# Kernel optimization log

Measured on AMD Instinct MI355X. Metric: run time of the kernel, lower is better.

## Reference

```python
import jax, jax.numpy as jnp
import numpy as np

HEADS = 8
DIM_HEAD = 64
DIM = 512
KERNEL = 33
SCALE = DIM_HEAD ** -0.5


def setup_inputs() -> dict:
    key = jax.random.key(0)
    k1, k2, k3, k4, k5, k6 = jax.random.split(key, 6)
    b, n = 2, 2048
    inner = HEADS * DIM_HEAD
    x = jax.random.normal(k1, (b, n, DIM), dtype=jnp.float32)
    mask = jax.random.uniform(k2, (b, n)) < 0.9
    W_qkv = jax.random.normal(k3, (DIM, inner * 3), dtype=jnp.float32) / np.sqrt(DIM)
    W_out = jax.random.normal(k4, (inner, DIM), dtype=jnp.float32) / np.sqrt(inner)
    b_out = jax.random.normal(k5, (DIM,), dtype=jnp.float32) * 0.01
    # depthwise Conv2d(heads, heads, (K,1), groups=heads) weight: (O=heads, I/groups=1, K, 1)
    conv_w = jax.random.normal(k6, (HEADS, 1, KERNEL, 1), dtype=jnp.float32) / np.sqrt(KERNEL)
    return {"x": x, "mask": mask, "W_qkv": W_qkv, "W_out": W_out,
            "b_out": b_out, "conv_w": conv_w}


def reference(x, mask, W_qkv, W_out, b_out, conv_w):
    b, n, _ = x.shape
    h, d = HEADS, DIM_HEAD
    qkv = (x @ W_qkv).reshape(b, n, 3, h, d)          # chunk(3) then (h d) split
    q = qkv[:, :, 0].transpose(0, 2, 1, 3)            # b h n d
    k = qkv[:, :, 1].transpose(0, 2, 1, 3)
    v = qkv[:, :, 2].transpose(0, 2, 1, 3)
    dots = jnp.einsum('bhid,bhjd->bhij', q, k) * SCALE
    mask_value = -jnp.finfo(dots.dtype).max
    dots = jnp.where(mask[:, None, None, :], dots, mask_value)
    attn = jax.nn.softmax(dots, axis=-1)
    out = jnp.einsum('bhij,bhjd->bhid', attn, v)      # b h n d
    # depthwise residual conv over sequence axis (height), per head
    pad = KERNEL // 2
    res = jax.lax.conv_general_dilated(
        v, conv_w, window_strides=(1, 1), padding=((pad, pad), (0, 0)),
        dimension_numbers=('NCHW', 'OIHW', 'NCHW'), feature_group_count=h)
    out = out + res
    out = out.transpose(0, 2, 1, 3).reshape(b, n, h * d)  # b n (h d)
    out = out @ W_out + b_out
    out = jnp.where(mask[:, :, None], out, 0.0)
    return out
```

## Files before the change

kernel.cpp:

```cpp
#include <hip/hip_runtime.h>
#include <float.h>

#define BATCH 2
#define SEQ   2048
#define HEADS 8
#define DHEAD 64
#define DIMM  512
#define NQKV  1536
#define QK_SCALE 0.125f

#define QKV_ELEMS ((size_t)BATCH * HEADS * SEQ * DHEAD)

typedef __bf16 bf16x8 __attribute__((ext_vector_type(8)));
typedef float  f32x4  __attribute__((ext_vector_type(4)));

__device__ __forceinline__ unsigned short bfbits(float f) {
  __bf16 h = (__bf16)f;
  return *(unsigned short*)&h;
}
__device__ __forceinline__ float bf2f(unsigned short u) {
  return __uint_as_float((unsigned)u << 16);
}

__global__ __launch_bounds__(1024) void prep_mask(const void* __restrict__ mraw,
                                                  float* __restrict__ maskf,
                                                  unsigned* __restrict__ kmaxn) {
  __shared__ int f_bf16, f_f32, f_gt1, f_oddnz;
  const int t = threadIdx.x;
  if (t < 16) kmaxn[t] = 0u;
  if (t == 0) { f_bf16 = 0; f_f32 = 0; f_gt1 = 0; f_oddnz = 0; }
  __syncthreads();
  const unsigned int* w = (const unsigned int*)mraw;
  unsigned int v = w[t];
  if (v == 0x3f803f80u) f_bf16 = 1;
  if (v == 0x3f800000u) f_f32 = 1;
  if (v > 1u)           f_gt1 = 1;
  if ((t & 1) && v != 0u) f_oddnz = 1;
  __syncthreads();
  int mode;
  if (f_bf16)       mode = 4;
  else if (f_f32)   mode = 3;
  else if (f_gt1)   mode = 1;
  else if (!f_oddnz) mode = 2;
  else              mode = 0;
  for (int i = t; i < BATCH * SEQ; i += 1024) {
    bool keep;
    if (mode == 4)      keep = ((const unsigned short*)mraw)[i] != 0;
    else if (mode == 3) keep = ((const float*)mraw)[i] != 0.f;
    else if (mode == 1) keep = ((const unsigned char*)mraw)[i] != 0;
    else if (mode == 2) keep = w[2 * i] != 0u;
    else                keep = w[i] != 0u;
    maskf[i] = keep ? 1.f : 0.f;
  }
}

__global__ __launch_bounds__(256) void transpose_w(const float* __restrict__ W,
                                                   unsigned short* __restrict__ Wt,
                                                   int K, int N) {
  __shared__ float T[64][65];
  const int t = threadIdx.x;
  const int n0 = blockIdx.x * 64, k0 = blockIdx.y * 64;
  {
    int r0 = t >> 4, c4 = t & 15;
#pragma unroll
    for (int rr = 0; rr < 4; ++rr) {
      int r = r0 + rr * 16;
      float4 v = *(const float4*)(W + (size_t)(k0 + r) * N + n0 + c4 * 4);
      T[r][c4 * 4 + 0] = v.x; T[r][c4 * 4 + 1] = v.y;
      T[r][c4 * 4 + 2] = v.z; T[r][c4 * 4 + 3] = v.w;
    }
  }
  __syncthreads();
  {
    int n = t >> 2, kc = t & 3;
    union { unsigned short u[16]; int4 v[2]; } p;
#pragma unroll
    for (int i = 0; i < 16; ++i) p.u[i] = bfbits(T[kc * 16 + i][n]);
    int4* dst = (int4*)(Wt + (size_t)(n0 + n) * K + k0 + kc * 16);
    dst[0] = p.v[0]; dst[1] = p.v[1];
  }
}

__global__ __launch_bounds__(256) void gemm_qkv_mfma(
    const float* __restrict__ X, const unsigned short* __restrict__ Wt,
    unsigned short* __restrict__ Qbf, unsigned short* __restrict__ Kbf,
    unsigned short* __restrict__ Vt) {
  __shared__ __align__(16) unsigned char Al[128 * 128];
  __shared__ __align__(16) unsigned char Bl[64 * 128];
  const int tid = threadIdx.x;
  const int lane = tid & 63;
  const int w = tid >> 6;
  const int l15 = lane & 15, g = lane >> 4;
  const int wr = w >> 1, wc = w & 1;
  int bid = blockIdx.x;
  int lid = (bid & 7) * 96 + (bid >> 3);
  int by = lid / 24, bx = lid - by * 24;
  const int m0 = by * 128;

  f32x4 acc[4][2] = {};
  const int srow = tid >> 3, scg = tid & 7;
  const int rsw = (l15 & 7) << 4;

  for (int k0 = 0; k0 < DIMM; k0 += 64) {
    __syncthreads();
#pragma unroll
    for (int it = 0; it < 4; ++it) {
      int row = srow + it * 32;
      int sw = (row & 7) << 4;
      const float* asrc = X + (size_t)(m0 + row) * DIMM + k0 + scg * 8;
      float4 a0 = *(const float4*)asrc;
      float4 a1 = *(const float4*)(asrc + 4);
      union { unsigned short u[8]; int4 v; } pk;
      pk.u[0] = bfbits(a0.x); pk.u[1] = bfbits(a0.y);
      pk.u[2] = bfbits(a0.z); pk.u[3] = bfbits(a0.w);
      pk.u[4] = bfbits(a1.x); pk.u[5] = bfbits(a1.y);
      pk.u[6] = bfbits(a1.z); pk.u[7] = bfbits(a1.w);
      *(int4*)(Al + row * 128 + ((scg * 16) ^ sw)) = pk.v;
      if (it < 2) {
        *(int4*)(Bl + row * 128 + ((scg * 16) ^ sw)) =
            *(const int4*)(Wt + (size_t)(bx * 64 + row) * DIMM + k0 + scg * 8);
      }
    }
    __syncthreads();
#pragma unroll
    for (int ks = 0; ks < 2; ++ks) {
      bf16x8 af[4], bfr[2];
#pragma unroll
      for (int mi = 0; mi < 4; ++mi)
        af[mi] = *(const bf16x8*)(Al + (wr * 64 + mi * 16 + l15) * 128 +
                                  ((ks * 64 + g * 16) ^ rsw));
#pragma unroll
      for (int nj = 0; nj < 2; ++nj)
        bfr[nj] = *(const bf16x8*)(Bl + (wc * 32 + nj * 16 + l15) * 128 +
                                   ((ks * 64 + g * 16) ^ rsw));
#pragma unroll
      for (int mi = 0; mi < 4; ++mi)
#pragma unroll
        for (int nj = 0; nj < 2; ++nj)
          acc[mi][nj] = __builtin_amdgcn_mfma_f32_16x16x32_bf16(
              af[mi], bfr[nj], acc[mi][nj], 0, 0, 0);
    }
  }
  const int chunk = bx >> 3;
  const int bb = m0 >> 11;
#pragma unroll
  for (int nj = 0; nj < 2; ++nj) {
    int col = (bx & 7) * 64 + wc * 32 + nj * 16 + l15;
    int hh = col >> 6, dd = col & 63;
#pragma unroll
    for (int mi = 0; mi < 4; ++mi) {
      int ii0 = (m0 & (SEQ - 1)) + wr * 64 + mi * 16 + g * 4;
      if (chunk == 2) {
        union { unsigned short u[4]; ushort4 v; } pk;
#pragma unroll
        for (int r = 0; r < 4; ++r) pk.u[r] = bfbits(acc[mi][nj][r]);
        *(ushort4*)(Vt + ((size_t)(bb * HEADS + hh) * DHEAD + dd) * SEQ + ii0) = pk.v;
      } else {
        unsigned short* dst = (chunk == 0) ? Qbf : Kbf;
        float sc = (chunk == 0) ? QK_SCALE : 1.f;
#pragma unroll
        for (int r = 0; r < 4; ++r)
          dst[((size_t)(bb * HEADS + hh) * SEQ + ii0 + r) * DHEAD + dd] =
              bfbits(acc[mi][nj][r] * sc);
      }
    }
  }
}

__global__ __launch_bounds__(256) void knorm(const unsigned short* __restrict__ Kbf,
                                             unsigned* __restrict__ kmaxn) {
  int row = blockIdx.x * 256 + threadIdx.x;
  const bf16x8* kr = (const bf16x8*)(Kbf + (size_t)row * DHEAD);
  float n2 = 0.f;
#pragma unroll
  for (int c = 0; c < 8; ++c) {
    bf16x8 v = kr[c];
#pragma unroll
    for (int i = 0; i < 8; ++i) { float f = (float)v[i]; n2 += f * f; }
  }
#pragma unroll
  for (int d = 1; d < 64; d <<= 1) n2 = fmaxf(n2, __shfl_xor(n2, d));
  if ((threadIdx.x & 63) == 0)
    atomicMax(kmaxn + (row >> 11), __float_as_uint(n2));
}

__global__ __launch_bounds__(256) void attn_split(const unsigned short* __restrict__ Qbf,
                                                  const unsigned short* __restrict__ Kbf,
                                                  const unsigned short* __restrict__ Vt,
                                                  const float* __restrict__ maskf,
                                                  const unsigned* __restrict__ kmaxn,
                                                  unsigned short* __restrict__ Po,
                                                  float* __restrict__ LSE) {
  __shared__ __align__(16) unsigned char Ks[8192];
  __shared__ __align__(16) unsigned char Vs[8192];
  __shared__ __align__(16) unsigned char Ps[8192];
  __shared__ float skm[64];
  __shared__ float qns[64];

  const int tid = threadIdx.x;
  const int lane = tid & 63;
  const int w = tid >> 6;
  const int l15 = lane & 15, g = lane >> 4;

  int fid = blockIdx.x;
  int lid = (fid & 7) * 128 + (fid >> 3);
  const int bh = lid >> 6;
  const int rem = lid & 63;
  const int qb = rem >> 1;
  const int half = rem & 1;
  const int bb = bh >> 3;

  const unsigned short* Qg = Qbf + ((size_t)bh * SEQ + qb * 64) * DHEAD;
  const unsigned short* Kg = Kbf + (size_t)bh * SEQ * DHEAD;
  const unsigned short* Vg = Vt  + (size_t)bh * DHEAD * SEQ;

  bf16x8 qf0, qf1;
  {
    const unsigned char* qrow = (const unsigned char*)(Qg + (size_t)(w * 16 + l15) * DHEAD);
    qf0 = *(const bf16x8*)(qrow + g * 16);
    qf1 = *(const bf16x8*)(qrow + 64 + g * 16);
  }
  {
    float qn2 = 0.f;
#pragma unroll
    for (int i = 0; i < 8; ++i) {
      float a = (float)qf0[i]; qn2 += a * a;
      float b = (float)qf1[i]; qn2 += b * b;
    }
    qn2 += __shfl_xor(qn2, 16);
    qn2 += __shfl_xor(qn2, 32);
    if (g == 0) qns[w * 16 + l15] = qn2;
  }
  __syncthreads();
  const float kmax2 = __uint_as_float(kmaxn[bh]);
  float B[4];
#pragma unroll
  for (int r = 0; r < 4; ++r) B[r] = sqrtf(qns[w * 16 + g * 4 + r] * kmax2);

  f32x4 o[4];
  float lsum[4] = {0.f, 0.f, 0.f, 0.f};
#pragma unroll
  for (int j = 0; j < 4; ++j) { o[j] = (f32x4){0.f, 0.f, 0.f, 0.f}; }

  const int sm = tid >> 2;
  const int sc = (tid & 3) * 32;
  const int ssw = (sm & 7) << 4;
  const int rsw = (l15 & 7) << 4;

  const int kt0 = half * 16;
  for (int kt = kt0; kt < kt0 + 16; ++kt) {
    __syncthreads();
    {
      const unsigned char* ksrc =
          (const unsigned char*)(Kg + (size_t)kt * 64 * DHEAD) + sm * 128 + sc;
      const unsigned char* vsrc =
          (const unsigned char*)(Vg + (size_t)sm * SEQ + kt * 64) + sc;
      *(int4*)(Ks + sm * 128 + ((sc)      ^ ssw)) = *(const int4*)(ksrc);
      *(int4*)(Ks + sm * 128 + ((sc + 16) ^ ssw)) = *(const int4*)(ksrc + 16);
      *(int4*)(Vs + sm * 128 + ((sc)      ^ ssw)) = *(const int4*)(vsrc);
      *(int4*)(Vs + sm * 128 + ((sc + 16) ^ ssw)) = *(const int4*)(vsrc + 16);
      if (tid < 64) skm[tid] = maskf[bb * SEQ + kt * 64 + tid];
    }
    __syncthreads();

    f32x4 s[4];
#pragma unroll
    for (int j = 0; j < 4; ++j) {
      const unsigned char* krow = Ks + (16 * j + l15) * 128;
      bf16x8 kf0 = *(const bf16x8*)(krow + ((g * 16)      ^ rsw));
      bf16x8 kf1 = *(const bf16x8*)(krow + ((64 + g * 16) ^ rsw));
      f32x4 z = (f32x4){0.f, 0.f, 0.f, 0.f};
      z = __builtin_amdgcn_mfma_f32_16x16x32_bf16(qf0, kf0, z, 0, 0, 0);
      z = __builtin_amdgcn_mfma_f32_16x16x32_bf16(qf1, kf1, z, 0, 0, 0);
      s[j] = z;
    }

    float km0 = skm[l15], km1 = skm[16 + l15], km2 = skm[32 + l15], km3 = skm[48 + l15];
#pragma unroll
    for (int r = 0; r < 4; ++r) {
      float p0 = __expf(s[0][r] - B[r]) * km0;
      float p1 = __expf(s[1][r] - B[r]) * km1;
      float p2 = __expf(s[2][r] - B[r]) * km2;
      float p3 = __expf(s[3][r] - B[r]) * km3;
      lsum[r] += (p0 + p1) + (p2 + p3);
      int pm = w * 16 + g * 4 + r;
      unsigned char* prow = Ps + pm * 128;
      int psw = (pm & 7) << 4;
      *(__bf16*)(prow + ((2 * (l15)      ) ^ psw)) = (__bf16)p0;
      *(__bf16*)(prow + ((2 * (16 + l15) ) ^ psw)) = (__bf16)p1;
      *(__bf16*)(prow + ((2 * (32 + l15) ) ^ psw)) = (__bf16)p2;
      *(__bf16*)(prow + ((2 * (48 + l15) ) ^ psw)) = (__bf16)p3;
    }

    {
      const unsigned char* parow = Ps + (w * 16 + l15) * 128;
      bf16x8 pa0 = *(const bf16x8*)(parow + ((g * 16)      ^ rsw));
      bf16x8 pa1 = *(const bf16x8*)(parow + ((64 + g * 16) ^ rsw));
#pragma unroll
      for (int j = 0; j < 4; ++j) {
        const unsigned char* vrow = Vs + (16 * j + l15) * 128;
        bf16x8 vf0 = *(const bf16x8*)(vrow + ((g * 16)      ^ rsw));
        bf16x8 vf1 = *(const bf16x8*)(vrow + ((64 + g * 16) ^ rsw));
        o[j] = __builtin_amdgcn_mfma_f32_16x16x32_bf16(pa0, vf0, o[j], 0, 0, 0);
        o[j] = __builtin_amdgcn_mfma_f32_16x16x32_bf16(pa1, vf1, o[j], 0, 0, 0);
      }
    }
  }

#pragma unroll
  for (int r = 0; r < 4; ++r) {
    float l = lsum[r];
    l += __shfl_xor(l, 1);
    l += __shfl_xor(l, 2);
    l += __shfl_xor(l, 4);
    l += __shfl_xor(l, 8);
    float inv = (l > 0.f) ? 1.f / l : 0.f;
    int row = qb * 64 + w * 16 + g * 4 + r;
    size_t base = half * QKV_ELEMS + ((size_t)bh * SEQ + row) * DHEAD + l15;
    Po[base]      = bfbits(o[0][r] * inv);
    Po[base + 16] = bfbits(o[1][r] * inv);
    Po[base + 32] = bfbits(o[2][r] * inv);
    Po[base + 48] = bfbits(o[3][r] * inv);
    if (l15 == 0)
      LSE[half * (BATCH * HEADS * SEQ) + bh * SEQ + row] =
          (l > 0.f) ? B[r] + __logf(l) : -3.0e38f;
  }
}

__global__ __launch_bounds__(256) void combine_conv(
    const unsigned short* __restrict__ Po, const float* __restrict__ LSE,
    const unsigned short* __restrict__ Vt, const float* __restrict__ cw,
    unsigned short* __restrict__ Obf) {
  __shared__ float T[96][68];
  __shared__ float cwl[33];
  const int tid = threadIdx.x;
  const int bid = blockIdx.x;
  const int bh = bid >> 5;
  const int n0 = (bid & 31) * 64;
  const int hh = bh & 7;
  if (tid < 33) cwl[tid] = cw[hh * 33 + tid];
  for (int idx = tid; idx < 64 * 24; idx += 256) {
    int d = idx / 24, c4 = idx - (idx / 24) * 24;
    int nbase = n0 - 16 + c4 * 4;
    const unsigned short* src = Vt + ((size_t)bh * DHEAD + d) * SEQ;
#pragma unroll
    for (int q = 0; q < 4; ++q) {
      int n = nbase + q;
      T[c4 * 4 + q][d] = (n >= 0 && n < SEQ) ? bf2f(src[n]) : 0.f;
    }
  }
  __syncthreads();
#pragma unroll
  for (int p = 0; p < 4; ++p) {
    int n = (tid >> 4) + p * 16;
    int d4 = tid & 15;
    int row = bh * SEQ + n0 + n;
    float ls0 = LSE[row], ls1 = LSE[BATCH * HEADS * SEQ + row];
    float m = fmaxf(ls0, ls1);
    float w0 = __expf(ls0 - m), w1 = __expf(ls1 - m);
    float inv = 1.f / (w0 + w1);
    w0 *= inv; w1 *= inv;
    const unsigned short* p0 = Po + (size_t)row * DHEAD + d4 * 4;
    const unsigned short* p1 = p0 + QKV_ELEMS;
    ushort4 a = *(const ushort4*)p0, b = *(const ushort4*)p1;
    float o0 = w0 * bf2f(a.x) + w1 * bf2f(b.x);
    float o1 = w0 * bf2f(a.y) + w1 * bf2f(b.y);
    float o2 = w0 * bf2f(a.z) + w1 * bf2f(b.z);
    float o3 = w0 * bf2f(a.w) + w1 * bf2f(b.w);
#pragma unroll
    for (int t = 0; t < 33; ++t) {
      float wv = cwl[t];
      float4 tv = *(const float4*)&T[n + t][d4 * 4];
      o0 += wv * tv.x; o1 += wv * tv.y; o2 += wv * tv.z; o3 += wv * tv.w;
    }
    union { unsigned short u[4]; ushort4 v; } pk;
    pk.u[0] = bfbits(o0); pk.u[1] = bfbits(o1);
    pk.u[2] = bfbits(o2); pk.u[3] = bfbits(o3);
    *(ushort4*)(Obf + (size_t)row * DHEAD + d4 * 4) = pk.v;
  }
}

__global__ __launch_bounds__(256) void gemm_out_mfma(
    const unsigned short* __restrict__ Obf, const unsigned short* __restrict__ Wt,
    const float* __restrict__ bias, const float* __restrict__ maskf,
    float* __restrict__ out) {
  __shared__ __align__(16) unsigned char Al[64 * 128];
  __shared__ __align__(16) unsigned char Bl[64 * 128];
  const int tid = threadIdx.x;
  const int lane = tid & 63;
  const int w = tid >> 6;
  const int l15 = lane & 15, g = lane >> 4;
  const int wr = w >> 1, wc = w & 1;
  int bid = blockIdx.x;
  int lid = (bid & 7) * 64 + (bid >> 3);
  int by = lid >> 3, bx = lid & 7;
  const int m0 = by * 64, n0 = bx * 64;
  const int bb = m0 >> 11;
  const int ii0 = m0 & (SEQ - 1);

  f32x4 acc[2][2] = {};
  const int srow = tid >> 3, scg = tid & 7;
  const int rsw = (l15 & 7) << 4;

  for (int k0 = 0; k0 < DIMM; k0 += 64) {
    const int hh = k0 >> 6;
    __syncthreads();
#pragma unroll
    for (int it = 0; it < 2; ++it) {
      int row = srow + it * 32;
      int sw = (row & 7) << 4;
      *(int4*)(Al + row * 128 + ((scg * 16) ^ sw)) =
          *(const int4*)(Obf + ((size_t)(bb * HEADS + hh) * SEQ + ii0 + row) * DHEAD + scg * 8);
      *(int4*)(Bl + row * 128 + ((scg * 16) ^ sw)) =
          *(const int4*)(Wt + (size_t)(n0 + row) * DIMM + k0 + scg * 8);
    }
    __syncthreads();
#pragma unroll
    for (int ks = 0; ks < 2; ++ks) {
      bf16x8 af[2], bfr[2];
#pragma unroll
      for (int mi = 0; mi < 2; ++mi)
        af[mi] = *(const bf16x8*)(Al + (wr * 32 + mi * 16 + l15) * 128 +
                                  ((ks * 64 + g * 16) ^ rsw));
#pragma unroll
      for (int nj = 0; nj < 2; ++nj)
        bfr[nj] = *(const bf16x8*)(Bl + (wc * 32 + nj * 16 + l15) * 128 +
                                   ((ks * 64 + g * 16) ^ rsw));
#pragma unroll
      for (int mi = 0; mi < 2; ++mi)
#pragma unroll
        for (int nj = 0; nj < 2; ++nj)
          acc[mi][nj] = __builtin_amdgcn_mfma_f32_16x16x32_bf16(
              af[mi], bfr[nj], acc[mi][nj], 0, 0, 0);
    }
  }
#pragma unroll
  for (int nj = 0; nj < 2; ++nj) {
    int col = n0 + wc * 32 + nj * 16 + l15;
    float bcol = bias[col];
#pragma unroll
    for (int mi = 0; mi < 2; ++mi) {
#pragma unroll
      for (int r = 0; r < 4; ++r) {
        int m = m0 + wr * 32 + mi * 16 + g * 4 + r;
        out[(size_t)m * DIMM + col] = (acc[mi][nj][r] + bcol) * maskf[m];
      }
    }
  }
}

extern "C" void kernel_launch(void* const* d_in, const int* in_sizes, int n_in,
                              void* d_out, int out_size, void* d_ws, size_t ws_size,
                              hipStream_t stream) {
  const float* x     = (const float*)d_in[0];
  const void*  mask  = d_in[1];
  const float* Wqkv  = (const float*)d_in[2];
  const float* Wout  = (const float*)d_in[3];
  const float* bout  = (const float*)d_in[4];
  const float* convw = (const float*)d_in[5];
  float* out = (float*)d_out;

  float* maskf = (float*)d_ws;
  unsigned* kmaxn = (unsigned*)(maskf + 4096);
  unsigned short* Qbf = (unsigned short*)(kmaxn + 64);
  unsigned short* Kbf = Qbf + QKV_ELEMS;
  unsigned short* Vt  = Kbf + QKV_ELEMS;
  unsigned short* Po  = Vt + QKV_ELEMS;
  float* LSE          = (float*)(Po + 2 * QKV_ELEMS);
  unsigned short* Obf = (unsigned short*)(LSE + 2 * BATCH * HEADS * SEQ);
  unsigned short* Wtq = Obf + QKV_ELEMS;
  unsigned short* Wto = Wtq + (size_t)NQKV * DIMM;

  prep_mask<<<1, 1024, 0, stream>>>(mask, maskf, kmaxn);
  transpose_w<<<dim3(NQKV / 64, DIMM / 64), 256, 0, stream>>>(Wqkv, Wtq, DIMM, NQKV);
  transpose_w<<<dim3(DIMM / 64, DIMM / 64), 256, 0, stream>>>(Wout, Wto, DIMM, DIMM);
  gemm_qkv_mfma<<<768, 256, 0, stream>>>(x, Wtq, Qbf, Kbf, Vt);
  knorm<<<(BATCH * HEADS * SEQ) / 256, 256, 0, stream>>>(Kbf, kmaxn);
  attn_split<<<1024, 256, 0, stream>>>(Qbf, Kbf, Vt, maskf, kmaxn, Po, LSE);
  combine_conv<<<512, 256, 0, stream>>>(Po, LSE, Vt, convw, Obf);
  gemm_out_mfma<<<512, 256, 0, stream>>>(Obf, Wto, bout, maskf, out);
}
```

Measured before the change: 109.3 us.

## Keep softmax probabilities in registers, prefetch K/V tiles, and pre-convert X to bf16

The attention kernel now computes S^T (K as the A operand) so that the exp'd probabilities land in the MFMA operand layout. They are packed with v_cvt_pk_bf16 and fed straight into 16x16x16 MFMAs, which removes the LDS round-trip for P and its extra barriers. Q is prescaled by log2(e) so exp2 can be used, the per-row bound is computed without shared memory, and the next K/V tile is prefetched into registers while the current one is processed. X is also converted to bf16 by a separate kernel before the QKV GEMM, which adds a launch and an extra buffer but halves the GEMM's A-operand load traffic.

```diff
diff --git a/kernel.cpp b/kernel.cpp
--- a/kernel.cpp
+++ b/kernel.cpp
@@ -8,11 +8,19 @@
 #define DIMM  512
 #define NQKV  1536
 #define QK_SCALE 0.125f
+#define QSCALE_L2 (0.125f * 1.44269504f)
 
 #define QKV_ELEMS ((size_t)BATCH * HEADS * SEQ * DHEAD)
 
 typedef __bf16 bf16x8 __attribute__((ext_vector_type(8)));
+typedef short  s16x4  __attribute__((ext_vector_type(4)));
 typedef float  f32x4  __attribute__((ext_vector_type(4)));
+
+#if __has_builtin(__builtin_amdgcn_exp2f)
+#define EXP2F __builtin_amdgcn_exp2f
+#else
+#define EXP2F exp2f
+#endif
 
 __device__ __forceinline__ unsigned short bfbits(float f) {
   __bf16 h = (__bf16)f;
@@ -20,6 +28,20 @@
 }
 __device__ __forceinline__ float bf2f(unsigned short u) {
   return __uint_as_float((unsigned)u << 16);
+}
+__device__ __forceinline__ unsigned cvtpk(float a, float b) {
+  unsigned r;
+  asm("v_cvt_pk_bf16_f32 %0, %1, %2" : "=v"(r) : "v"(a), "v"(b));
+  return r;
+}
+__device__ __forceinline__ f32x4 mfma16(s16x4 a, s16x4 b, f32x4 c) {
+#if __has_builtin(__builtin_amdgcn_mfma_f32_16x16x16bf16_1k)
+  return __builtin_amdgcn_mfma_f32_16x16x16bf16_1k(a, b, c, 0, 0, 0);
+#else
+  f32x4 d;
+  asm("v_mfma_f32_16x16x16_bf16 %0, %1, %2, %3" : "=v"(d) : "v"(a), "v"(b), "v"(c));
+  return d;
+#endif
 }
 
 __global__ __launch_bounds__(1024) void prep_mask(const void* __restrict__ mraw,
@@ -54,6 +76,19 @@
   }
 }
 
+__global__ __launch_bounds__(256) void x_to_bf16(const float* __restrict__ X,
+                                                 unsigned short* __restrict__ Xbf) {
+  size_t i = ((size_t)blockIdx.x * 256 + threadIdx.x) * 8;
+  float4 a0 = *(const float4*)(X + i);
+  float4 a1 = *(const float4*)(X + i + 4);
+  union { unsigned short u[8]; int4 v; } pk;
+  pk.u[0] = bfbits(a0.x); pk.u[1] = bfbits(a0.y);
+  pk.u[2] = bfbits(a0.z); pk.u[3] = bfbits(a0.w);
+  pk.u[4] = bfbits(a1.x); pk.u[5] = bfbits(a1.y);
+  pk.u[6] = bfbits(a1.z); pk.u[7] = bfbits(a1.w);
+  *(int4*)(Xbf + i) = pk.v;
+}
+
 __global__ __launch_bounds__(256) void transpose_w(const float* __restrict__ W,
                                                    unsigned short* __restrict__ Wt,
                                                    int K, int N) {
@@ -82,7 +117,7 @@
 }
 
 __global__ __launch_bounds__(256) void gemm_qkv_mfma(
-    const float* __restrict__ X, const unsigned short* __restrict__ Wt,
+    const unsigned short* __restrict__ Xbf, const unsigned short* __restrict__ Wt,
     unsigned short* __restrict__ Qbf, unsigned short* __restrict__ Kbf,
     unsigned short* __restrict__ Vt) {
   __shared__ __align__(16) unsigned char Al[128 * 128];
@@ -107,15 +142,8 @@
     for (int it = 0; it < 4; ++it) {
       int row = srow + it * 32;
       int sw = (row & 7) << 4;
-      const float* asrc = X + (size_t)(m0 + row) * DIMM + k0 + scg * 8;
-      float4 a0 = *(const float4*)asrc;
-      float4 a1 = *(const float4*)(asrc + 4);
-      union { unsigned short u[8]; int4 v; } pk;
-      pk.u[0] = bfbits(a0.x); pk.u[1] = bfbits(a0.y);
-      pk.u[2] = bfbits(a0.z); pk.u[3] = bfbits(a0.w);
-      pk.u[4] = bfbits(a1.x); pk.u[5] = bfbits(a1.y);
-      pk.u[6] = bfbits(a1.z); pk.u[7] = bfbits(a1.w);
-      *(int4*)(Al + row * 128 + ((scg * 16) ^ sw)) = pk.v;
+      *(int4*)(Al + row * 128 + ((scg * 16) ^ sw)) =
+          *(const int4*)(Xbf + (size_t)(m0 + row) * DIMM + k0 + scg * 8);
       if (it < 2) {
         *(int4*)(Bl + row * 128 + ((scg * 16) ^ sw)) =
             *(const int4*)(Wt + (size_t)(bx * 64 + row) * DIMM + k0 + scg * 8);
@@ -157,7 +185,7 @@
         *(ushort4*)(Vt + ((size_t)(bb * HEADS + hh) * DHEAD + dd) * SEQ + ii0) = pk.v;
       } else {
         unsigned short* dst = (chunk == 0) ? Qbf : Kbf;
-        float sc = (chunk == 0) ? QK_SCALE : 1.f;
+        float sc = (chunk == 0) ? QSCALE_L2 : 1.f;
 #pragma unroll
         for (int r = 0; r < 4; ++r)
           dst[((size_t)(bb * HEADS + hh) * SEQ + ii0 + r) * DHEAD + dd] =
@@ -193,9 +221,7 @@
                                                   float* __restrict__ LSE) {
   __shared__ __align__(16) unsigned char Ks[8192];
   __shared__ __align__(16) unsigned char Vs[8192];
-  __shared__ __align__(16) unsigned char Ps[8192];
-  __shared__ float skm[64];
-  __shared__ float qns[64];
+  __shared__ __align__(16) float skm[64];
 
   const int tid = threadIdx.x;
   const int lane = tid & 63;
@@ -220,6 +246,7 @@
     qf0 = *(const bf16x8*)(qrow + g * 16);
     qf1 = *(const bf16x8*)(qrow + 64 + g * 16);
   }
+  float Bx, Bnat;
   {
     float qn2 = 0.f;
 #pragma unroll
@@ -229,18 +256,13 @@
     }
     qn2 += __shfl_xor(qn2, 16);
     qn2 += __shfl_xor(qn2, 32);
-    if (g == 0) qns[w * 16 + l15] = qn2;
-  }
-  __syncthreads();
-  const float kmax2 = __uint_as_float(kmaxn[bh]);
-  float B[4];
-#pragma unroll
-  for (int r = 0; r < 4; ++r) B[r] = sqrtf(qns[w * 16 + g * 4 + r] * kmax2);
-
-  f32x4 o[4];
-  float lsum[4] = {0.f, 0.f, 0.f, 0.f};
-#pragma unroll
-  for (int j = 0; j < 4; ++j) { o[j] = (f32x4){0.f, 0.f, 0.f, 0.f}; }
+    const float kmax2 = __uint_as_float(kmaxn[bh]);
+    Bx = sqrtf(qn2 * kmax2);
+    Bnat = Bx * 0.69314718f;
+  }
+
+  f32x4 o[4] = {};
+  float lsum = 0.f;
 
   const int sm = tid >> 2;
   const int sc = (tid & 3) * 32;
@@ -248,18 +270,33 @@
   const int rsw = (l15 & 7) << 4;
 
   const int kt0 = half * 16;
+  int4 rk0, rk1, rv0, rv1;
+  float rmv = 0.f;
+  {
+    const unsigned char* ksrc =
+        (const unsigned char*)(Kg + (size_t)kt0 * 64 * DHEAD) + sm * 128 + sc;
+    const unsigned char* vsrc =
+        (const unsigned char*)(Vg + (size_t)sm * SEQ + kt0 * 64) + sc;
+    rk0 = *(const int4*)(ksrc); rk1 = *(const int4*)(ksrc + 16);
+    rv0 = *(const int4*)(vsrc); rv1 = *(const int4*)(vsrc + 16);
+    if (tid < 64) rmv = maskf[bb * SEQ + kt0 * 64 + tid];
+  }
+
   for (int kt = kt0; kt < kt0 + 16; ++kt) {
     __syncthreads();
-    {
+    *(int4*)(Ks + sm * 128 + ((sc)      ^ ssw)) = rk0;
+    *(int4*)(Ks + sm * 128 + ((sc + 16) ^ ssw)) = rk1;
+    *(int4*)(Vs + sm * 128 + ((sc)      ^ ssw)) = rv0;
+    *(int4*)(Vs + sm * 128 + ((sc + 16) ^ ssw)) = rv1;
+    if (tid < 64) skm[tid] = rmv;
+    if (kt + 1 < kt0 + 16) {
       const unsigned char* ksrc =
-          (const unsigned char*)(Kg + (size_t)kt * 64 * DHEAD) + sm * 128 + sc;
+          (const unsigned char*)(Kg + (size_t)(kt + 1) * 64 * DHEAD) + sm * 128 + sc;
       const unsigned char* vsrc =
-          (const unsigned char*)(Vg + (size_t)sm * SEQ + kt * 64) + sc;
-      *(int4*)(Ks + sm * 128 + ((sc)      ^ ssw)) = *(const int4*)(ksrc);
-      *(int4*)(Ks + sm * 128 + ((sc + 16) ^ ssw)) = *(const int4*)(ksrc + 16);
-      *(int4*)(Vs + sm * 128 + ((sc)      ^ ssw)) = *(const int4*)(vsrc);
-      *(int4*)(Vs + sm * 128 + ((sc + 16) ^ ssw)) = *(const int4*)(vsrc + 16);
-      if (tid < 64) skm[tid] = maskf[bb * SEQ + kt * 64 + tid];
+          (const unsigned char*)(Vg + (size_t)sm * SEQ + (kt + 1) * 64) + sc;
+      rk0 = *(const int4*)(ksrc); rk1 = *(const int4*)(ksrc + 16);
+      rv0 = *(const int4*)(vsrc); rv1 = *(const int4*)(vsrc + 16);
+      if (tid < 64) rmv = maskf[bb * SEQ + (kt + 1) * 64 + tid];
     }
     __syncthreads();
 
@@ -270,60 +307,54 @@
       bf16x8 kf0 = *(const bf16x8*)(krow + ((g * 16)      ^ rsw));
       bf16x8 kf1 = *(const bf16x8*)(krow + ((64 + g * 16) ^ rsw));
       f32x4 z = (f32x4){0.f, 0.f, 0.f, 0.f};
-      z = __builtin_amdgcn_mfma_f32_16x16x32_bf16(qf0, kf0, z, 0, 0, 0);
-      z = __builtin_amdgcn_mfma_f32_16x16x32_bf16(qf1, kf1, z, 0, 0, 0);
+      z = __builtin_amdgcn_mfma_f32_16x16x32_bf16(kf0, qf0, z, 0, 0, 0);
+      z = __builtin_amdgcn_mfma_f32_16x16x32_bf16(kf1, qf1, z, 0, 0, 0);
       s[j] = z;
     }
 
-    float km0 = skm[l15], km1 = skm[16 + l15], km2 = skm[32 + l15], km3 = skm[48 + l15];
-#pragma unroll
-    for (int r = 0; r < 4; ++r) {
-      float p0 = __expf(s[0][r] - B[r]) * km0;
-      float p1 = __expf(s[1][r] - B[r]) * km1;
-      float p2 = __expf(s[2][r] - B[r]) * km2;
-      float p3 = __expf(s[3][r] - B[r]) * km3;
-      lsum[r] += (p0 + p1) + (p2 + p3);
-      int pm = w * 16 + g * 4 + r;
-      unsigned char* prow = Ps + pm * 128;
-      int psw = (pm & 7) << 4;
-      *(__bf16*)(prow + ((2 * (l15)      ) ^ psw)) = (__bf16)p0;
-      *(__bf16*)(prow + ((2 * (16 + l15) ) ^ psw)) = (__bf16)p1;
-      *(__bf16*)(prow + ((2 * (32 + l15) ) ^ psw)) = (__bf16)p2;
-      *(__bf16*)(prow + ((2 * (48 + l15) ) ^ psw)) = (__bf16)p3;
-    }
-
-    {
-      const unsigned char* parow = Ps + (w * 16 + l15) * 128;
-      bf16x8 pa0 = *(const bf16x8*)(parow + ((g * 16)      ^ rsw));
-      bf16x8 pa1 = *(const bf16x8*)(parow + ((64 + g * 16) ^ rsw));
+    s16x4 pa[4];
+#pragma unroll
+    for (int j = 0; j < 4; ++j) {
+      float4 km4 = *(const float4*)&skm[16 * j + 4 * g];
+      float p0 = EXP2F(s[j][0] - Bx) * km4.x;
+      float p1 = EXP2F(s[j][1] - Bx) * km4.y;
+      float p2 = EXP2F(s[j][2] - Bx) * km4.z;
+      float p3 = EXP2F(s[j][3] - Bx) * km4.w;
+      lsum += (p0 + p1) + (p2 + p3);
+      union { uint2 u; s16x4 v; } pk;
+      pk.u.x = cvtpk(p0, p1);
+      pk.u.y = cvtpk(p2, p3);
+      pa[j] = pk.v;
+    }
+
+#pragma unroll
+    for (int dj = 0; dj < 4; ++dj) {
+      const unsigned char* vrow = Vs + (16 * dj + l15) * 128;
 #pragma unroll
       for (int j = 0; j < 4; ++j) {
-        const unsigned char* vrow = Vs + (16 * j + l15) * 128;
-        bf16x8 vf0 = *(const bf16x8*)(vrow + ((g * 16)      ^ rsw));
-        bf16x8 vf1 = *(const bf16x8*)(vrow + ((64 + g * 16) ^ rsw));
-        o[j] = __builtin_amdgcn_mfma_f32_16x16x32_bf16(pa0, vf0, o[j], 0, 0, 0);
-        o[j] = __builtin_amdgcn_mfma_f32_16x16x32_bf16(pa1, vf1, o[j], 0, 0, 0);
+        s16x4 vb = *(const s16x4*)(vrow + ((32 * j + 8 * g) ^ rsw));
+        o[dj] = mfma16(pa[j], vb, o[dj]);
       }
     }
   }
 
+  lsum += __shfl_xor(lsum, 16);
+  lsum += __shfl_xor(lsum, 32);
 #pragma unroll
   for (int r = 0; r < 4; ++r) {
-    float l = lsum[r];
-    l += __shfl_xor(l, 1);
-    l += __shfl_xor(l, 2);
-    l += __shfl_xor(l, 4);
-    l += __shfl_xor(l, 8);
-    float inv = (l > 0.f) ? 1.f / l : 0.f;
-    int row = qb * 64 + w * 16 + g * 4 + r;
+    float lr = __shfl(lsum, 4 * g + r);
+    float inv = (lr > 0.f) ? 1.f / lr : 0.f;
+    int row = qb * 64 + w * 16 + 4 * g + r;
     size_t base = half * QKV_ELEMS + ((size_t)bh * SEQ + row) * DHEAD + l15;
     Po[base]      = bfbits(o[0][r] * inv);
     Po[base + 16] = bfbits(o[1][r] * inv);
     Po[base + 32] = bfbits(o[2][r] * inv);
     Po[base + 48] = bfbits(o[3][r] * inv);
-    if (l15 == 0)
-      LSE[half * (BATCH * HEADS * SEQ) + bh * SEQ + row] =
-          (l > 0.f) ? B[r] + __logf(l) : -3.0e38f;
+  }
+  if (g == 0) {
+    int row = qb * 64 + w * 16 + l15;
+    LSE[half * (BATCH * HEADS * SEQ) + bh * SEQ + row] =
+        (lsum > 0.f) ? Bnat + __logf(lsum) : -3.0e38f;
   }
 }
 
@@ -470,11 +501,13 @@
   unsigned short* Obf = (unsigned short*)(LSE + 2 * BATCH * HEADS * SEQ);
   unsigned short* Wtq = Obf + QKV_ELEMS;
   unsigned short* Wto = Wtq + (size_t)NQKV * DIMM;
+  unsigned short* Xbf = Wto + (size_t)DIMM * DIMM;
 
   prep_mask<<<1, 1024, 0, stream>>>(mask, maskf, kmaxn);
+  x_to_bf16<<<1024, 256, 0, stream>>>(x, Xbf);
   transpose_w<<<dim3(NQKV / 64, DIMM / 64), 256, 0, stream>>>(Wqkv, Wtq, DIMM, NQKV);
   transpose_w<<<dim3(DIMM / 64, DIMM / 64), 256, 0, stream>>>(Wout, Wto, DIMM, DIMM);
-  gemm_qkv_mfma<<<768, 256, 0, stream>>>(x, Wtq, Qbf, Kbf, Vt);
+  gemm_qkv_mfma<<<768, 256, 0, stream>>>(Xbf, Wtq, Qbf, Kbf, Vt);
   knorm<<<(BATCH * HEADS * SEQ) / 256, 256, 0, stream>>>(Kbf, kmaxn);
   attn_split<<<1024, 256, 0, stream>>>(Qbf, Kbf, Vt, maskf, kmaxn, Po, LSE);
   combine_conv<<<512, 256, 0, stream>>>(Po, LSE, Vt, convw, Obf);
```

Result: faster. 102.0 us (-6.7%).
